# Kernel tuning notes

Measured on AMD Instinct MI355X. Metric: run time of the kernel, lower is better.

The kernel has to match this reference:

```python
import jax, jax.numpy as jnp
import numpy as np

SEQ, BATCH, IN_DIM, HID, LAYERS, OUT = 512, 64, 512, 1024, 4, 1


def setup_inputs() -> dict:
    key = jax.random.key(0)
    ks = jax.random.split(key, 8)
    s = 1.0 / np.sqrt(HID)  # PyTorch default init range
    u = lambda k, shape: jax.random.uniform(k, shape, jnp.float32, -s, s)
    return {
        "x": jax.random.normal(ks[0], (SEQ, BATCH, IN_DIM), jnp.float32),
        "w_ih0": u(ks[1], (4 * HID, IN_DIM)),
        "w_ih_rest": u(ks[2], (LAYERS - 1, 4 * HID, HID)),
        "w_hh": u(ks[3], (LAYERS, 4 * HID, HID)),
        "b_ih": u(ks[4], (LAYERS, 4 * HID)),
        "b_hh": u(ks[5], (LAYERS, 4 * HID)),
        "fc_w": u(ks[6], (OUT, HID)),
        "fc_b": u(ks[7], (OUT,)),
    }


def _lstm_layer(xs, w_ih, w_hh, b):
    # xs: [T, B, D]; PyTorch gate order: i, f, g, o
    T, B, _ = xs.shape
    H = w_hh.shape[1]
    gx = jnp.einsum("tbd,gd->tbg", xs, w_ih) + b  # precompute input GEMM [T,B,4H]

    def step(carry, g_t):
        h, c = carry
        g = g_t + h @ w_hh.T
        i, f, gg, o = jnp.split(g, 4, axis=-1)
        c = jax.nn.sigmoid(f) * c + jax.nn.sigmoid(i) * jnp.tanh(gg)
        h = jax.nn.sigmoid(o) * jnp.tanh(c)
        return (h, c), h

    init = (jnp.zeros((B, H), xs.dtype), jnp.zeros((B, H), xs.dtype))
    _, hs = jax.lax.scan(step, init, gx)
    return hs  # [T, B, H]


def reference(x, w_ih0, w_ih_rest, w_hh, b_ih, b_hh, fc_w, fc_b):
    h = _lstm_layer(x, w_ih0, w_hh[0], b_ih[0] + b_hh[0])
    for l in range(1, LAYERS):
        h = _lstm_layer(h, w_ih_rest[l - 1], w_hh[l], b_ih[l] + b_hh[l])
    # Faithful to original: output is seq-first [T,B,H], and x[:, -1, :]
    # selects the LAST BATCH element over all timesteps -> [T, H]
    last = jax.nn.sigmoid(h[:, -1, :])
    return last @ fc_w.T + fc_b  # [T, OUT]
```

## Files before the change

kernel.cpp:

```cpp
#include <hip/hip_runtime.h>


typedef unsigned short u16;
typedef short bf16x8 __attribute__((ext_vector_type(8)));
typedef float f32x4 __attribute__((ext_vector_type(4)));
typedef float f32x16 __attribute__((ext_vector_type(16)));

__device__ __forceinline__ u16 f2bf(float f) {
  unsigned u = __float_as_uint(f);
  return (u16)((u + 0x7FFFu + ((u >> 16) & 1u)) >> 16);
}
__device__ __forceinline__ float bf2f(u16 s) {
  return __uint_as_float(((unsigned)s) << 16);
}
__device__ __forceinline__ bf16x8 ld8(const u16* p) {
  uint4 v = *(const uint4*)p;
  return __builtin_bit_cast(bf16x8, v);
}
__device__ __forceinline__ float sigf(float x) {
  x = fminf(fmaxf(x, -30.f), 30.f);
  return 1.f / (1.f + __expf(-x));
}
__device__ __forceinline__ float tanhf_(float x) {
  x = fminf(fmaxf(x, -15.f), 15.f);
  float e = __expf(-2.f * x);
  return (1.f - e) / (1.f + e);
}

#define AT_LD(p) __hip_atomic_load((p), __ATOMIC_RELAXED, __HIP_MEMORY_SCOPE_AGENT)
#define AT_ST(p, v) __hip_atomic_store((p), (v), __ATOMIC_RELAXED, __HIP_MEMORY_SCOPE_AGENT)

__global__ void repack_w(const float* __restrict__ wih0, const float* __restrict__ wihr,
                         const float* __restrict__ whh, u16* __restrict__ WCAT) {
  size_t i = (size_t)blockIdx.x * 256 + threadIdx.x;
  int l = (int)(i >> 23);
  int r = (int)(i >> 11) & 4095;
  int c = (int)i & 2047;
  int Kx = l ? 1024 : 512;
  float v = 0.f;
  if (c < Kx) v = l ? wihr[((size_t)(l - 1) * 4096 + r) * 1024 + c]
                    : wih0[(size_t)r * 512 + c];
  else if (c < Kx + 1024) v = whh[((size_t)l * 4096 + r) * 1024 + (c - Kx)];
  WCAT[i] = f2bf(v);
}

__global__ void repack_x(const float* __restrict__ x, u16* __restrict__ XP) {
  int i = blockIdx.x * 256 + threadIdx.x;
  int t = i >> 12, r = i & 4095, kc = r >> 6, b = r & 63;
  const float* src = x + ((size_t)t * 64 + b) * 512 + kc * 8;
  float4 v0 = *(const float4*)src, v1 = *(const float4*)(src + 4);
  u16 o[8] = {f2bf(v0.x), f2bf(v0.y), f2bf(v0.z), f2bf(v0.w),
              f2bf(v1.x), f2bf(v1.y), f2bf(v1.z), f2bf(v1.w)};
  *(uint4*)(XP + ((size_t)(t * 64 + kc) * 64 + b) * 8) = *(uint4*)o;
}

__global__ void bias_add(const float* __restrict__ a, const float* __restrict__ b,
                         float* __restrict__ o) {
  int i = blockIdx.x * blockDim.x + threadIdx.x;
  o[i] = a[i] + b[i];
}

template <int NF, int FX>
__device__ __forceinline__ void run_pipe(
    int layer, int w64, const u16* __restrict__ WCAT, const u16* __restrict__ XP,
    u16* __restrict__ HR, u16* __restrict__ HOUT, const float* __restrict__ BIAS,
    unsigned* __restrict__ FLAG, unsigned* __restrict__ EPOCH, float* R) {
  const int tid = threadIdx.x;
  const int lane = tid & 63, wv = tid >> 6;
  const int ks = wv & 3, nh = wv >> 2;
  const int l31 = lane & 31, lhi = lane >> 5;
  const int W = layer * 64 + w64;

  bf16x8 wf[NF];
  {
    const int lr = nh * 32 + l31;
    const int grow = (lr >> 4) * 1024 + 16 * w64 + (lr & 15);
    const u16* wrow = WCAT + ((size_t)layer * 4096 + grow) * 2048;
#pragma unroll
    for (int kk = 0; kk < NF; ++kk) {
      int f = ks * NF + kk;
      wf[kk] = ld8(wrow + f * 16 + lhi * 8);
    }
  }

  const int u = tid & 15, bp = tid >> 4;
  const int col = 16 * w64 + u;
  float c0 = 0.f, c1 = 0.f;
  const float bi = BIAS[layer * 4096 + col];
  const float bf_ = BIAS[layer * 4096 + 1024 + col];
  const float bg = BIAS[layer * 4096 + 2048 + col];
  const float bo = BIAS[layer * 4096 + 3072 + col];

  const int lane_base = (lhi * 64 + l31) * 8;
  u16* HRL = HR + (size_t)layer * 2097152;
  const u16* M0B = (NF == 32) ? HR + (size_t)(layer - 1) * 2097152 : XP;
  const int lrD = nh * 32 + l31;

  for (int s = 0; s < 515; ++s) {
    const int t = s - layer;
    const bool active = (t >= 0) && (t < 512);
    if (active) {
      *(f32x4*)&R[tid * 8] = f32x4{0.f, 0.f, 0.f, 0.f};
      *(f32x4*)&R[tid * 8 + 4] = f32x4{0.f, 0.f, 0.f, 0.f};
      __syncthreads();

      const u16* P0 = M0B + ((NF == 32) ? (size_t)(t & 31) * 65536
                                        : (size_t)t * 32768) + lane_base;
      const u16* P1 = HRL + (size_t)((t - 1) & 31) * 65536 + lane_base - (size_t)FX * 1024;

      f32x16 acc0 = {}, acc1 = {};
      uint4 a0[4], a1[4];
#pragma unroll
      for (int p = 0; p < 4; ++p) {
        int f = ks * NF + p;
        const u16* ap = (f < FX ? P0 : P1) + (size_t)f * 1024;
        a0[p] = *(const uint4*)ap;
        a1[p] = *(const uint4*)(ap + 256);
      }
#pragma unroll
      for (int kk = 0; kk < NF; ++kk) {
        uint4 ca = a0[kk & 3], cb = a1[kk & 3];
        if (kk + 4 < NF) {
          int f = ks * NF + kk + 4;
          const u16* ap = (f < FX ? P0 : P1) + (size_t)f * 1024;
          a0[kk & 3] = *(const uint4*)ap;
          a1[kk & 3] = *(const uint4*)(ap + 256);
        }
        acc0 = __builtin_amdgcn_mfma_f32_32x32x16_bf16(
            __builtin_bit_cast(bf16x8, ca), wf[kk], acc0, 0, 0, 0);
        acc1 = __builtin_amdgcn_mfma_f32_32x32x16_bf16(
            __builtin_bit_cast(bf16x8, cb), wf[kk], acc1, 0, 0, 0);
      }
#pragma unroll
      for (int r = 0; r < 16; ++r) {
        int m = (r & 3) + 8 * (r >> 2) + 4 * lhi;
        atomicAdd(&R[m * 64 + lrD], acc0[r]);
        atomicAdd(&R[(32 + m) * 64 + lrD], acc1[r]);
      }
      __syncthreads();
      {
        float p0i = R[bp * 64 + u] + bi, p0f = R[bp * 64 + 16 + u] + bf_;
        float p0g = R[bp * 64 + 32 + u] + bg, p0o = R[bp * 64 + 48 + u] + bo;
        float p1i = R[(bp + 32) * 64 + u] + bi, p1f = R[(bp + 32) * 64 + 16 + u] + bf_;
        float p1g = R[(bp + 32) * 64 + 32 + u] + bg, p1o = R[(bp + 32) * 64 + 48 + u] + bo;
        c0 = sigf(p0f) * c0 + sigf(p0i) * tanhf_(p0g);
        float h0 = sigf(p0o) * tanhf_(c0);
        c1 = sigf(p1f) * c1 + sigf(p1i) * tanhf_(p1g);
        float h1 = sigf(p1o) * tanhf_(c1);
        u16 hb0 = f2bf(h0), hb1 = f2bf(h1);
        unsigned n0 = (unsigned)(u16)__shfl_down((int)(unsigned)hb0, 1, 64);
        unsigned n1 = (unsigned)(u16)__shfl_down((int)(unsigned)hb1, 1, 64);
        if ((u & 1) == 0) {
          unsigned pk0 = (unsigned)hb0 | (n0 << 16);
          unsigned pk1 = (unsigned)hb1 | (n1 << 16);
          u16* slot = HRL + (size_t)(t & 31) * 65536;
          size_t e0 = ((size_t)(col >> 3) * 64 + bp) * 8 + (col & 7);
          AT_ST((unsigned*)(slot + e0), pk0);
          AT_ST((unsigned*)(slot + e0 + 256), pk1);
          if (layer == 3 && bp == 31)
            *(unsigned*)(HOUT + (size_t)t * 1024 + col) = pk1;
        }
      }
      __syncthreads();
    }
    const unsigned tgt = (unsigned)(s + 1);
    if (tid == 0) AT_ST(&FLAG[W * 64], tgt);
    if (W == 0) {
      if (wv == 0) {
        for (;;) {
          unsigned f0 = AT_LD(&FLAG[lane * 64]);
          unsigned f1 = AT_LD(&FLAG[(lane + 64) * 64]);
          unsigned f2 = AT_LD(&FLAG[(lane + 128) * 64]);
          unsigned f3 = AT_LD(&FLAG[(lane + 192) * 64]);
          bool ok = (f0 >= tgt) & (f1 >= tgt) & (f2 >= tgt) & (f3 >= tgt);
          if (__ballot(ok) == ~0ull) break;
          __builtin_amdgcn_s_sleep(1);
        }
        if (lane < 32) AT_ST(&EPOCH[lane * 64], tgt);
      }
    } else if (wv == 0) {
      unsigned* ep = &EPOCH[(W & 31) * 64];
      while (AT_LD(ep) < tgt) __builtin_amdgcn_s_sleep(1);
    }
    __syncthreads();
  }
}

__global__ __launch_bounds__(512, 2) void lstm_pipe(
    const u16* __restrict__ WCAT, const u16* __restrict__ XP,
    u16* __restrict__ HR, u16* __restrict__ HOUT,
    const float* __restrict__ BIAS, unsigned* __restrict__ FLAG,
    unsigned* __restrict__ EPOCH) {
  __shared__ float R[64 * 64];
  const int w = blockIdx.x;
  const int layer = w >> 6, w64 = w & 63;
  if (layer == 0) run_pipe<24, 32>(0, w64, WCAT, XP, HR, HOUT, BIAS, FLAG, EPOCH, R);
  else            run_pipe<32, 64>(layer, w64, WCAT, XP, HR, HOUT, BIAS, FLAG, EPOCH, R);
}

__global__ void lstm_head(const u16* __restrict__ Hl, const float* __restrict__ fcw,
                          const float* __restrict__ fcb, float* __restrict__ out) {
  int t = blockIdx.x, tid = threadIdx.x;
  const u16* hrow = Hl + (size_t)t * 1024;
  float s = 0.f;
  for (int j = tid; j < 1024; j += 256)
    s += sigf(bf2f(hrow[j])) * fcw[j];
  for (int o = 32; o; o >>= 1) s += __shfl_down(s, o, 64);
  __shared__ float red[4];
  if ((tid & 63) == 0) red[tid >> 6] = s;
  __syncthreads();
  if (tid == 0) out[t] = red[0] + red[1] + red[2] + red[3] + fcb[0];
}

extern "C" void kernel_launch(void* const* d_in, const int* in_sizes, int n_in,
                              void* d_out, int out_size, void* d_ws, size_t ws_size,
                              hipStream_t stream) {
  const float* x    = (const float*)d_in[0];
  const float* wih0 = (const float*)d_in[1];
  const float* wihr = (const float*)d_in[2];
  const float* whh  = (const float*)d_in[3];
  const float* bih  = (const float*)d_in[4];
  const float* bhh  = (const float*)d_in[5];
  const float* fcw  = (const float*)d_in[6];
  const float* fcb  = (const float*)d_in[7];
  float* out = (float*)d_out;

  char* ws = (char*)d_ws;
  size_t off = 0;
  auto alc = [&](size_t b) { void* p = ws + off; off = (off + b + 255) & ~(size_t)255; return p; };
  u16* WCAT  = (u16*)alc(33554432ull * 2);
  u16* XP    = (u16*)alc(16777216ull * 2);
  u16* HR    = (u16*)alc(8388608ull * 2);
  u16* HOUT  = (u16*)alc(524288ull * 2);
  float* BIAS = (float*)alc(16384 * 4);
  unsigned* FLAG  = (unsigned*)alc(256 * 64 * 4);
  unsigned* EPOCH = (unsigned*)alc(32 * 64 * 4);
  (void)ws_size; (void)in_sizes; (void)n_in; (void)out_size;

  hipMemsetAsync(HR, 0, 8388608ull * 2, stream);
  hipMemsetAsync(FLAG, 0, 256 * 64 * 4, stream);
  hipMemsetAsync(EPOCH, 0, 32 * 64 * 4, stream);
  repack_w<<<dim3(131072), 256, 0, stream>>>(wih0, wihr, whh, WCAT);
  repack_x<<<dim3(8192), 256, 0, stream>>>(x, XP);
  bias_add<<<dim3(64), 256, 0, stream>>>(bih, bhh, BIAS);

  void* args[] = {&WCAT, &XP, &HR, &HOUT, &BIAS, &FLAG, &EPOCH};
  hipLaunchCooperativeKernel((const void*)lstm_pipe, dim3(256), dim3(512),
                             args, 0, stream);

  lstm_head<<<dim3(512), 256, 0, stream>>>(HOUT, fcw, fcb, out);
}
```

Baseline: 14.84 ms.

## Replace global barrier with per-dependency flag waits in LSTM wavefront pipeline

Drops the grid-wide epoch barrier driven by block 0, where every block waited on every other block each step. Each block now polls only the flags of its producers: the previous layer at t+1, its own layer at t, and the next layer within the 32-slot ring window. It also double-buffers the LDS reduction tile, so the zeroing for the next step folds into the current step and one __syncthreads goes away. The A-operand prefetch depth grows from 4 to 8, which costs more registers and adds polling traffic from 64 lanes per block.

```diff
diff --git a/kernel.cpp b/kernel.cpp
--- a/kernel.cpp
+++ b/kernel.cpp
@@ -64,7 +64,7 @@
 __device__ __forceinline__ void run_pipe(
     int layer, int w64, const u16* __restrict__ WCAT, const u16* __restrict__ XP,
     u16* __restrict__ HR, u16* __restrict__ HOUT, const float* __restrict__ BIAS,
-    unsigned* __restrict__ FLAG, unsigned* __restrict__ EPOCH, float* R) {
+    int* __restrict__ FLAG, float* R) {
   const int tid = threadIdx.x;
   const int lane = tid & 63, wv = tid >> 6;
   const int ks = wv & 3, nh = wv >> 2;
@@ -96,106 +96,107 @@
   const u16* M0B = (NF == 32) ? HR + (size_t)(layer - 1) * 2097152 : XP;
   const int lrD = nh * 32 + l31;
 
-  for (int s = 0; s < 515; ++s) {
-    const int t = s - layer;
-    const bool active = (t >= 0) && (t < 512);
-    if (active) {
-      *(f32x4*)&R[tid * 8] = f32x4{0.f, 0.f, 0.f, 0.f};
-      *(f32x4*)&R[tid * 8 + 4] = f32x4{0.f, 0.f, 0.f, 0.f};
-      __syncthreads();
-
-      const u16* P0 = M0B + ((NF == 32) ? (size_t)(t & 31) * 65536
-                                        : (size_t)t * 32768) + lane_base;
-      const u16* P1 = HRL + (size_t)((t - 1) & 31) * 65536 + lane_base - (size_t)FX * 1024;
-
-      f32x16 acc0 = {}, acc1 = {};
-      uint4 a0[4], a1[4];
-#pragma unroll
-      for (int p = 0; p < 4; ++p) {
-        int f = ks * NF + p;
+  const bool needA = (layer > 0) && (ks * NF < FX);
+  const bool needB = (ks * NF + NF > FX);
+  const bool needC = (layer < 3);
+  const int lm1 = (layer > 0) ? layer - 1 : layer;
+  const int lp1 = (layer < 3) ? layer + 1 : layer;
+  int* fA = FLAG + (lm1 * 64 + lane) * 64;
+  int* fB = FLAG + (layer * 64 + lane) * 64;
+  int* fC = FLAG + (lp1 * 64 + lane) * 64;
+  const int NEVER = -0x40000000;
+
+  *(f32x4*)&R[tid * 8] = f32x4{0.f, 0.f, 0.f, 0.f};
+  *(f32x4*)&R[tid * 8 + 4] = f32x4{0.f, 0.f, 0.f, 0.f};
+  __syncthreads();
+
+  for (int t = 0; t < 512; ++t) {
+    {
+      const int thA = needA ? t + 1 : NEVER;
+      const int thB = needB ? t : NEVER;
+      const int thC = needC ? t - 31 : NEVER;
+      for (;;) {
+        bool ok = (AT_LD(fA) >= thA) & (AT_LD(fB) >= thB) & (AT_LD(fC) >= thC);
+        if (__ballot(ok) == ~0ull) break;
+        __builtin_amdgcn_s_sleep(1);
+      }
+    }
+
+    float* Rb = R + (t & 1) * 4096;
+    const u16* P0 = M0B + ((NF == 32) ? (size_t)(t & 31) * 65536
+                                      : (size_t)t * 32768) + lane_base;
+    const u16* P1 = HRL + (size_t)((t - 1) & 31) * 65536 + lane_base - (size_t)FX * 1024;
+
+    f32x16 acc0 = {}, acc1 = {};
+    uint4 a0[8], a1[8];
+#pragma unroll
+    for (int p = 0; p < 8; ++p) {
+      int f = ks * NF + p;
+      const u16* ap = (f < FX ? P0 : P1) + (size_t)f * 1024;
+      a0[p] = *(const uint4*)ap;
+      a1[p] = *(const uint4*)(ap + 256);
+    }
+#pragma unroll
+    for (int kk = 0; kk < NF; ++kk) {
+      uint4 ca = a0[kk & 7], cb = a1[kk & 7];
+      if (kk + 8 < NF) {
+        int f = ks * NF + kk + 8;
         const u16* ap = (f < FX ? P0 : P1) + (size_t)f * 1024;
-        a0[p] = *(const uint4*)ap;
-        a1[p] = *(const uint4*)(ap + 256);
+        a0[kk & 7] = *(const uint4*)ap;
+        a1[kk & 7] = *(const uint4*)(ap + 256);
       }
-#pragma unroll
-      for (int kk = 0; kk < NF; ++kk) {
-        uint4 ca = a0[kk & 3], cb = a1[kk & 3];
-        if (kk + 4 < NF) {
-          int f = ks * NF + kk + 4;
-          const u16* ap = (f < FX ? P0 : P1) + (size_t)f * 1024;
-          a0[kk & 3] = *(const uint4*)ap;
-          a1[kk & 3] = *(const uint4*)(ap + 256);
-        }
-        acc0 = __builtin_amdgcn_mfma_f32_32x32x16_bf16(
-            __builtin_bit_cast(bf16x8, ca), wf[kk], acc0, 0, 0, 0);
-        acc1 = __builtin_amdgcn_mfma_f32_32x32x16_bf16(
-            __builtin_bit_cast(bf16x8, cb), wf[kk], acc1, 0, 0, 0);
+      acc0 = __builtin_amdgcn_mfma_f32_32x32x16_bf16(
+          __builtin_bit_cast(bf16x8, ca), wf[kk], acc0, 0, 0, 0);
+      acc1 = __builtin_amdgcn_mfma_f32_32x32x16_bf16(
+          __builtin_bit_cast(bf16x8, cb), wf[kk], acc1, 0, 0, 0);
+    }
+#pragma unroll
+    for (int r = 0; r < 16; ++r) {
+      int m = (r & 3) + 8 * (r >> 2) + 4 * lhi;
+      atomicAdd(&Rb[m * 64 + lrD], acc0[r]);
+      atomicAdd(&Rb[(32 + m) * 64 + lrD], acc1[r]);
+    }
+    __syncthreads();
+    {
+      float p0i = Rb[bp * 64 + u] + bi, p0f = Rb[bp * 64 + 16 + u] + bf_;
+      float p0g = Rb[bp * 64 + 32 + u] + bg, p0o = Rb[bp * 64 + 48 + u] + bo;
+      float p1i = Rb[(bp + 32) * 64 + u] + bi, p1f = Rb[(bp + 32) * 64 + 16 + u] + bf_;
+      float p1g = Rb[(bp + 32) * 64 + 32 + u] + bg, p1o = Rb[(bp + 32) * 64 + 48 + u] + bo;
+      c0 = sigf(p0f) * c0 + sigf(p0i) * tanhf_(p0g);
+      float h0 = sigf(p0o) * tanhf_(c0);
+      c1 = sigf(p1f) * c1 + sigf(p1i) * tanhf_(p1g);
+      float h1 = sigf(p1o) * tanhf_(c1);
+      u16 hb0 = f2bf(h0), hb1 = f2bf(h1);
+      unsigned n0 = (unsigned)(u16)__shfl_down((int)(unsigned)hb0, 1, 64);
+      unsigned n1 = (unsigned)(u16)__shfl_down((int)(unsigned)hb1, 1, 64);
+      if ((u & 1) == 0) {
+        unsigned pk0 = (unsigned)hb0 | (n0 << 16);
+        unsigned pk1 = (unsigned)hb1 | (n1 << 16);
+        u16* slot = HRL + (size_t)(t & 31) * 65536;
+        size_t e0 = ((size_t)(col >> 3) * 64 + bp) * 8 + (col & 7);
+        AT_ST((unsigned*)(slot + e0), pk0);
+        AT_ST((unsigned*)(slot + e0 + 256), pk1);
+        if (layer == 3 && bp == 31)
+          *(unsigned*)(HOUT + (size_t)t * 1024 + col) = pk1;
       }
-#pragma unroll
-      for (int r = 0; r < 16; ++r) {
-        int m = (r & 3) + 8 * (r >> 2) + 4 * lhi;
-        atomicAdd(&R[m * 64 + lrD], acc0[r]);
-        atomicAdd(&R[(32 + m) * 64 + lrD], acc1[r]);
-      }
-      __syncthreads();
-      {
-        float p0i = R[bp * 64 + u] + bi, p0f = R[bp * 64 + 16 + u] + bf_;
-        float p0g = R[bp * 64 + 32 + u] + bg, p0o = R[bp * 64 + 48 + u] + bo;
-        float p1i = R[(bp + 32) * 64 + u] + bi, p1f = R[(bp + 32) * 64 + 16 + u] + bf_;
-        float p1g = R[(bp + 32) * 64 + 32 + u] + bg, p1o = R[(bp + 32) * 64 + 48 + u] + bo;
-        c0 = sigf(p0f) * c0 + sigf(p0i) * tanhf_(p0g);
-        float h0 = sigf(p0o) * tanhf_(c0);
-        c1 = sigf(p1f) * c1 + sigf(p1i) * tanhf_(p1g);
-        float h1 = sigf(p1o) * tanhf_(c1);
-        u16 hb0 = f2bf(h0), hb1 = f2bf(h1);
-        unsigned n0 = (unsigned)(u16)__shfl_down((int)(unsigned)hb0, 1, 64);
-        unsigned n1 = (unsigned)(u16)__shfl_down((int)(unsigned)hb1, 1, 64);
-        if ((u & 1) == 0) {
-          unsigned pk0 = (unsigned)hb0 | (n0 << 16);
-          unsigned pk1 = (unsigned)hb1 | (n1 << 16);
-          u16* slot = HRL + (size_t)(t & 31) * 65536;
-          size_t e0 = ((size_t)(col >> 3) * 64 + bp) * 8 + (col & 7);
-          AT_ST((unsigned*)(slot + e0), pk0);
-          AT_ST((unsigned*)(slot + e0 + 256), pk1);
-          if (layer == 3 && bp == 31)
-            *(unsigned*)(HOUT + (size_t)t * 1024 + col) = pk1;
-        }
-      }
-      __syncthreads();
-    }
-    const unsigned tgt = (unsigned)(s + 1);
-    if (tid == 0) AT_ST(&FLAG[W * 64], tgt);
-    if (W == 0) {
-      if (wv == 0) {
-        for (;;) {
-          unsigned f0 = AT_LD(&FLAG[lane * 64]);
-          unsigned f1 = AT_LD(&FLAG[(lane + 64) * 64]);
-          unsigned f2 = AT_LD(&FLAG[(lane + 128) * 64]);
-          unsigned f3 = AT_LD(&FLAG[(lane + 192) * 64]);
-          bool ok = (f0 >= tgt) & (f1 >= tgt) & (f2 >= tgt) & (f3 >= tgt);
-          if (__ballot(ok) == ~0ull) break;
-          __builtin_amdgcn_s_sleep(1);
-        }
-        if (lane < 32) AT_ST(&EPOCH[lane * 64], tgt);
-      }
-    } else if (wv == 0) {
-      unsigned* ep = &EPOCH[(W & 31) * 64];
-      while (AT_LD(ep) < tgt) __builtin_amdgcn_s_sleep(1);
+      float* Rn = R + ((t + 1) & 1) * 4096;
+      *(f32x4*)&Rn[tid * 8] = f32x4{0.f, 0.f, 0.f, 0.f};
+      *(f32x4*)&Rn[tid * 8 + 4] = f32x4{0.f, 0.f, 0.f, 0.f};
     }
     __syncthreads();
+    if (tid == 0) AT_ST(&FLAG[W * 64], t + 1);
   }
 }
 
 __global__ __launch_bounds__(512, 2) void lstm_pipe(
     const u16* __restrict__ WCAT, const u16* __restrict__ XP,
     u16* __restrict__ HR, u16* __restrict__ HOUT,
-    const float* __restrict__ BIAS, unsigned* __restrict__ FLAG,
-    unsigned* __restrict__ EPOCH) {
-  __shared__ float R[64 * 64];
+    const float* __restrict__ BIAS, int* __restrict__ FLAG) {
+  __shared__ float R[2 * 4096];
   const int w = blockIdx.x;
   const int layer = w >> 6, w64 = w & 63;
-  if (layer == 0) run_pipe<24, 32>(0, w64, WCAT, XP, HR, HOUT, BIAS, FLAG, EPOCH, R);
-  else            run_pipe<32, 64>(layer, w64, WCAT, XP, HR, HOUT, BIAS, FLAG, EPOCH, R);
+  if (layer == 0) run_pipe<24, 32>(0, w64, WCAT, XP, HR, HOUT, BIAS, FLAG, R);
+  else            run_pipe<32, 64>(layer, w64, WCAT, XP, HR, HOUT, BIAS, FLAG, R);
 }
 
 __global__ void lstm_head(const u16* __restrict__ Hl, const float* __restrict__ fcw,
@@ -233,18 +234,16 @@
   u16* HR    = (u16*)alc(8388608ull * 2);
   u16* HOUT  = (u16*)alc(524288ull * 2);
   float* BIAS = (float*)alc(16384 * 4);
-  unsigned* FLAG  = (unsigned*)alc(256 * 64 * 4);
-  unsigned* EPOCH = (unsigned*)alc(32 * 64 * 4);
+  int* FLAG  = (int*)alc(256 * 64 * 4);
   (void)ws_size; (void)in_sizes; (void)n_in; (void)out_size;
 
   hipMemsetAsync(HR, 0, 8388608ull * 2, stream);
   hipMemsetAsync(FLAG, 0, 256 * 64 * 4, stream);
-  hipMemsetAsync(EPOCH, 0, 32 * 64 * 4, stream);
   repack_w<<<dim3(131072), 256, 0, stream>>>(wih0, wihr, whh, WCAT);
   repack_x<<<dim3(8192), 256, 0, stream>>>(x, XP);
   bias_add<<<dim3(64), 256, 0, stream>>>(bih, bhh, BIAS);
 
-  void* args[] = {&WCAT, &XP, &HR, &HOUT, &BIAS, &FLAG, &EPOCH};
+  void* args[] = {&WCAT, &XP, &HR, &HOUT, &BIAS, &FLAG};
   hipLaunchCooperativeKernel((const void*)lstm_pipe, dim3(256), dim3(512),
                              args, 0, stream);
 
```

Measured after the change: 15.37 ms. 3.6% more time.
